# Optimization experiments

Hardware: AMD Instinct MI355X
Metric: run time of the kernel (lower is better)

## Reference

```python
import jax, jax.numpy as jnp
import numpy as np

N_NODES = 25000
N_EDGES = 100000
NODE_IN = 8
EDGE_IN = 4
HID = 32


def _glorot(key, shape):
    fan_in, fan_out = shape[0], shape[-1]
    s = jnp.sqrt(2.0 / (fan_in + fan_out))
    return jax.random.normal(key, shape, dtype=jnp.float32) * s


def setup_inputs() -> dict:
    key = jax.random.key(0)
    ks = jax.random.split(key, 16)
    x = jax.random.normal(ks[0], (N_NODES, NODE_IN), dtype=jnp.float32)
    edge_index = jax.random.randint(ks[1], (2, N_EDGES), 0, N_NODES, dtype=jnp.int64)
    edge_attr = jax.random.uniform(ks[2], (N_EDGES, EDGE_IN), dtype=jnp.float32)
    params = {
        # conv1: edge MLP (edge_in -> node_in*hid), root lin (node_in->hid, no bias), bias
        'w_mlp1': _glorot(ks[3], (EDGE_IN, NODE_IN * HID)),
        'b_mlp1': jnp.zeros((NODE_IN * HID,), jnp.float32),
        'root1': _glorot(ks[4], (NODE_IN, HID)),
        'bias1': jnp.zeros((HID,), jnp.float32),
        # conv2
        'w_mlp2': _glorot(ks[5], (EDGE_IN, HID * HID)),
        'b_mlp2': jnp.zeros((HID * HID,), jnp.float32),
        'root2': _glorot(ks[6], (HID, HID)),
        'bias2': jnp.zeros((HID,), jnp.float32),
        # conv3
        'w_mlp3': _glorot(ks[7], (EDGE_IN, HID * HID)),
        'b_mlp3': jnp.zeros((HID * HID,), jnp.float32),
        'root3': _glorot(ks[8], (HID, HID)),
        'bias3': jnp.zeros((HID,), jnp.float32),
        # output head: Linear(hid,hid) -> ReLU -> Linear(hid,1)
        'w_out1': _glorot(ks[9], (HID, HID)),
        'b_out1': jnp.zeros((HID,), jnp.float32),
        'w_out2': _glorot(ks[10], (HID, 1)),
        'b_out2': jnp.zeros((1,), jnp.float32),
    }
    return {'x': x, 'edge_index': edge_index, 'edge_attr': edge_attr, **params}


def _nnconv(x, src, dst, edge_attr, w_mlp, b_mlp, root, bias, in_dim, out_dim, num_nodes):
    # edge MLP -> per-edge weight matrix [E, in, out]
    w_e = jax.nn.relu(edge_attr @ w_mlp + b_mlp).reshape(-1, in_dim, out_dim)
    # gather source features, per-edge matvec
    msg = jnp.einsum('ei,eio->eo', x[src], w_e)  # [E, out]
    # scatter-mean into target nodes
    agg = jax.ops.segment_sum(msg, dst, num_segments=num_nodes)
    cnt = jax.ops.segment_sum(jnp.ones((msg.shape[0],), msg.dtype), dst, num_segments=num_nodes)
    agg = agg / jnp.maximum(cnt, 1.0)[:, None]
    return agg + x @ root + bias


def reference(x, edge_index, edge_attr,
              w_mlp1, b_mlp1, root1, bias1,
              w_mlp2, b_mlp2, root2, bias2,
              w_mlp3, b_mlp3, root3, bias3,
              w_out1, b_out1, w_out2, b_out2):
    src, dst = edge_index[0], edge_index[1]
    n = x.shape[0]
    h = jax.nn.relu(_nnconv(x, src, dst, edge_attr, w_mlp1, b_mlp1, root1, bias1, NODE_IN, HID, n))
    h = jax.nn.relu(_nnconv(h, src, dst, edge_attr, w_mlp2, b_mlp2, root2, bias2, HID, HID, n))
    h = jax.nn.relu(_nnconv(h, src, dst, edge_attr, w_mlp3, b_mlp3, root3, bias3, HID, HID, n))
    h = jax.nn.relu(h @ w_out1 + b_out1)
    return h @ w_out2 + b_out2  # [N, 1]
```

## Files before the change

### kernel.cpp

```cpp
#include <hip/hip_runtime.h>

#define HID 32
#define CAP 64

__global__ __launch_bounds__(256) void build_kernel(
    const int* __restrict__ src, const int* __restrict__ dst,
    const float* __restrict__ ea,
    int* __restrict__ deg, int* __restrict__ perm_src, float4* __restrict__ perm_ea,
    int E)
{
    int e = blockIdx.x * blockDim.x + threadIdx.x;
    if (e >= E) return;
    int d = dst[e];
    int pos = atomicAdd(deg + d, 1) & (CAP - 1);
    size_t slot = (size_t)d * CAP + pos;
    perm_src[slot] = src[e];
    perm_ea[slot]  = *(const float4*)(ea + (size_t)e * 4);
}

__global__ __launch_bounds__(256) void pull8_kernel(
    const float* __restrict__ x,
    const int* __restrict__ deg,
    const int* __restrict__ perm_src, const float4* __restrict__ perm_ea,
    const float* __restrict__ w_mlp,
    const float* __restrict__ b_mlp,
    const float* __restrict__ root,
    const float* __restrict__ bias,
    float* __restrict__ h_out,
    int N)
{
    constexpr int IN = 8, NPG = 4;
    const int o = threadIdx.x & 31;
    const int g = (blockIdx.x * blockDim.x + threadIdx.x) >> 5;
    if (g >= (N + NPG - 1) / NPG) return;

    float wa[IN], wb[IN], wc[IN], wd[IN], br[IN], ro[IN];
    #pragma unroll
    for (int i = 0; i < IN; ++i) {
        int c = i * HID + o;
        wa[i] = w_mlp[c];
        wb[i] = w_mlp[IN * HID + c];
        wc[i] = w_mlp[2 * IN * HID + c];
        wd[i] = w_mlp[3 * IN * HID + c];
        br[i] = b_mlp[c];
        ro[i] = root[c];
    }
    const float bo = bias[o];

    #pragma unroll
    for (int nv = 0; nv < NPG; ++nv) {
        const int v = g * NPG + nv;
        if (v >= N) break;
        const int dg = min(deg[v], CAP);
        const int* ps = perm_src + (size_t)v * CAP;
        const float4* pe = perm_ea + (size_t)v * CAP;

        float acc = 0.f;
        if (dg > 0) {
            int sA = ps[0];
            float4 aA = pe[0];
            for (int k = 0; k < dg; ++k) {
                int sB = 0; float4 aB = make_float4(0.f, 0.f, 0.f, 0.f);
                if (k + 1 < dg) { sB = ps[k + 1]; aB = pe[k + 1]; }
                float4 x0 = *(const float4*)(x + (size_t)sA * IN);
                float4 x1 = *(const float4*)(x + (size_t)sA * IN + 4);
                const float xs[8] = { x0.x, x0.y, x0.z, x0.w, x1.x, x1.y, x1.z, x1.w };
                #pragma unroll
                for (int i = 0; i < IN; ++i) {
                    float t = fmaf(aA.x, wa[i], br[i]);
                    t = fmaf(aA.y, wb[i], t);
                    t = fmaf(aA.z, wc[i], t);
                    t = fmaf(aA.w, wd[i], t);
                    t = fmaxf(t, 0.f);
                    acc = fmaf(xs[i], t, acc);
                }
                sA = sB; aA = aB;
            }
        }
        float4 r0 = *(const float4*)(x + (size_t)v * IN);
        float4 r1 = *(const float4*)(x + (size_t)v * IN + 4);
        const float xr[8] = { r0.x, r0.y, r0.z, r0.w, r1.x, r1.y, r1.z, r1.w };
        float r = bo;
        #pragma unroll
        for (int i = 0; i < IN; ++i) r = fmaf(xr[i], ro[i], r);
        const float m = acc / fmaxf((float)dg, 1.f);
        h_out[(size_t)v * HID + o] = fmaxf(m + r, 0.f);
    }
}

template<bool HEAD>
__global__ __launch_bounds__(256) void pull32_kernel(
    const float* __restrict__ h_in,
    const int* __restrict__ deg,
    const int* __restrict__ perm_src, const float4* __restrict__ perm_ea,
    const float* __restrict__ w_mlp,
    const float* __restrict__ b_mlp,
    const float* __restrict__ root,
    const float* __restrict__ bias,
    const float* __restrict__ hw1, const float* __restrict__ hb1,
    const float* __restrict__ hw2, const float* __restrict__ hb2,
    float* __restrict__ h_out,
    int N)
{
    constexpr int IN = 32, IH = 16, NPW = 5;
    const int lane = threadIdx.x & 63;
    const int o    = lane & 31;
    const int half = lane >> 5;
    const int wave = (blockIdx.x * blockDim.x + threadIdx.x) >> 6;
    if (wave >= (N + NPW - 1) / NPW) return;

    float wa[IH], wb[IH], wc[IH], wd[IH], br[IH], ro[IH];
    #pragma unroll
    for (int i = 0; i < IH; ++i) {
        int c = (half * IH + i) * HID + o;
        wa[i] = w_mlp[c];
        wb[i] = w_mlp[IN * HID + c];
        wc[i] = w_mlp[2 * IN * HID + c];
        wd[i] = w_mlp[3 * IN * HID + c];
        br[i] = b_mlp[c];
        ro[i] = root[c];
    }
    const float bo = bias[o];

    #pragma unroll
    for (int nv = 0; nv < NPW; ++nv) {
        const int v = wave * NPW + nv;
        if (v >= N) break;
        const int dg = min(deg[v], CAP);
        const int* ps = perm_src + (size_t)v * CAP;
        const float4* pe = perm_ea + (size_t)v * CAP;

        float acc = 0.f;
        if (dg > 0) {
            int sA = ps[0];
            float4 aA = pe[0];
            for (int k = 0; k < dg; ++k) {
                int sB = 0; float4 aB = make_float4(0.f, 0.f, 0.f, 0.f);
                if (k + 1 < dg) { sB = ps[k + 1]; aB = pe[k + 1]; }
                const float* xp = h_in + (size_t)sA * IN + half * IH;
                float4 x0 = *(const float4*)(xp);
                float4 x1 = *(const float4*)(xp + 4);
                float4 x2 = *(const float4*)(xp + 8);
                float4 x3 = *(const float4*)(xp + 12);
                const float xs[16] = { x0.x, x0.y, x0.z, x0.w, x1.x, x1.y, x1.z, x1.w,
                                       x2.x, x2.y, x2.z, x2.w, x3.x, x3.y, x3.z, x3.w };
                #pragma unroll
                for (int i = 0; i < IH; ++i) {
                    float t = fmaf(aA.x, wa[i], br[i]);
                    t = fmaf(aA.y, wb[i], t);
                    t = fmaf(aA.z, wc[i], t);
                    t = fmaf(aA.w, wd[i], t);
                    t = fmaxf(t, 0.f);
                    acc = fmaf(xs[i], t, acc);
                }
                sA = sB; aA = aB;
            }
        }
        const float* rp = h_in + (size_t)v * IN + half * IH;
        float4 r0 = *(const float4*)(rp);
        float4 r1 = *(const float4*)(rp + 4);
        float4 r2 = *(const float4*)(rp + 8);
        float4 r3 = *(const float4*)(rp + 12);
        const float xr[16] = { r0.x, r0.y, r0.z, r0.w, r1.x, r1.y, r1.z, r1.w,
                               r2.x, r2.y, r2.z, r2.w, r3.x, r3.y, r3.z, r3.w };
        float rpart = 0.f;
        #pragma unroll
        for (int i = 0; i < IH; ++i) rpart = fmaf(xr[i], ro[i], rpart);

        const float dgf = fmaxf((float)dg, 1.f);
        float part = acc / dgf + rpart;
        part += __shfl_down(part, 32);

        if (lane < 32) {
            float h = fmaxf(part + bo, 0.f);
            if (!HEAD) {
                h_out[(size_t)v * HID + o] = h;
            } else {
                float t = hb1[o];
                #pragma unroll
                for (int i = 0; i < HID; ++i)
                    t = fmaf(__shfl(h, i, 32), hw1[i * HID + o], t);
                t = fmaxf(t, 0.f) * hw2[o];
                #pragma unroll
                for (int dd = 16; dd > 0; dd >>= 1)
                    t += __shfl_down(t, dd, 32);
                if (o == 0) h_out[v] = t + hb2[0];
            }
        }
    }
}

extern "C" void kernel_launch(void* const* d_in, const int* in_sizes, int n_in,
                              void* d_out, int out_size, void* d_ws, size_t ws_size,
                              hipStream_t stream)
{
    const float* x      = (const float*)d_in[0];
    const int*   ei     = (const int*)d_in[1];
    const float* ea     = (const float*)d_in[2];
    const float* w_mlp1 = (const float*)d_in[3];
    const float* b_mlp1 = (const float*)d_in[4];
    const float* root1  = (const float*)d_in[5];
    const float* bias1  = (const float*)d_in[6];
    const float* w_mlp2 = (const float*)d_in[7];
    const float* b_mlp2 = (const float*)d_in[8];
    const float* root2  = (const float*)d_in[9];
    const float* bias2  = (const float*)d_in[10];
    const float* w_mlp3 = (const float*)d_in[11];
    const float* b_mlp3 = (const float*)d_in[12];
    const float* root3  = (const float*)d_in[13];
    const float* bias3  = (const float*)d_in[14];
    const float* w_out1 = (const float*)d_in[15];
    const float* b_out1 = (const float*)d_in[16];
    const float* w_out2 = (const float*)d_in[17];
    const float* b_out2 = (const float*)d_in[18];

    const int NODE_IN = 8;
    const int N = in_sizes[0] / NODE_IN;
    const int E = in_sizes[2] / 4;
    const int* src = ei;
    const int* dst = ei + E;

    char* ws = (char*)d_ws;
    size_t off = 0;
    auto carve = [&](size_t bytes) {
        char* p = ws + off;
        off += (bytes + 255) & ~(size_t)255;
        return p;
    };
    int*    deg      = (int*)carve((size_t)N * 4);
    int*    perm_src = (int*)carve((size_t)N * CAP * 4);
    float4* perm_ea  = (float4*)carve((size_t)N * CAP * 16);
    float*  h1       = (float*)carve((size_t)N * HID * 4);
    float*  h2       = (float*)carve((size_t)N * HID * 4);
    float*  outp     = (float*)d_out;

    const int TB = 256;
    const int buildBlocks = (E + TB - 1) / TB;
    const int NPG = 4, NPW = 5;
    const int p8Blocks  = (((N + NPG - 1) / NPG) * 32 + TB - 1) / TB;
    const int p32Blocks = (((N + NPW - 1) / NPW) * 64 + TB - 1) / TB;

    hipMemsetAsync(deg, 0, (size_t)N * 4, stream);

    build_kernel<<<buildBlocks, TB, 0, stream>>>(src, dst, ea, deg, perm_src, perm_ea, E);

    pull8_kernel<<<p8Blocks, TB, 0, stream>>>(x, deg, perm_src, perm_ea,
                                              w_mlp1, b_mlp1, root1, bias1, h1, N);

    pull32_kernel<false><<<p32Blocks, TB, 0, stream>>>(h1, deg, perm_src, perm_ea,
                                                       w_mlp2, b_mlp2, root2, bias2,
                                                       nullptr, nullptr, nullptr, nullptr, h2, N);

    pull32_kernel<true><<<p32Blocks, TB, 0, stream>>>(h2, deg, perm_src, perm_ea,
                                                      w_mlp3, b_mlp3, root3, bias3,
                                                      w_out1, b_out1, w_out2, b_out2, outp, N);
}
```

Measured before the change: 244.3 us.

## Batch neighbor gathers four at a time and prefetch next node's edge slots

```diff
diff --git a/kernel.cpp b/kernel.cpp
--- a/kernel.cpp
+++ b/kernel.cpp
@@ -1,7 +1,7 @@
 #include <hip/hip_runtime.h>
 
 #define HID 32
-#define CAP 64
+#define CAP 32
 
 __global__ __launch_bounds__(256) void build_kernel(
     const int* __restrict__ src, const int* __restrict__ dst,
@@ -18,7 +18,7 @@
     perm_ea[slot]  = *(const float4*)(ea + (size_t)e * 4);
 }
 
-__global__ __launch_bounds__(256) void pull8_kernel(
+__global__ __launch_bounds__(256, 3) void pull8_kernel(
     const float* __restrict__ x,
     const int* __restrict__ deg,
     const int* __restrict__ perm_src, const float4* __restrict__ perm_ea,
@@ -30,9 +30,10 @@
     int N)
 {
     constexpr int IN = 8, NPG = 4;
-    const int o = threadIdx.x & 31;
-    const int g = (blockIdx.x * blockDim.x + threadIdx.x) >> 5;
-    if (g >= (N + NPG - 1) / NPG) return;
+    const int o  = threadIdx.x & 31;
+    const int g  = (blockIdx.x * blockDim.x + threadIdx.x) >> 5;
+    const int v0 = g * NPG;
+    if (v0 >= N) return;
 
     float wa[IN], wb[IN], wc[IN], wd[IN], br[IN], ro[IN];
     #pragma unroll
@@ -47,49 +48,113 @@
     }
     const float bo = bias[o];
 
+    int dgs[NPG];
+    #pragma unroll
+    for (int t = 0; t < NPG; ++t)
+        dgs[t] = (v0 + t < N) ? min(deg[v0 + t], CAP) : 0;
+
+    int4 s4A = *(const int4*)(perm_src + (size_t)v0 * CAP);
+    float4 aA0 = perm_ea[(size_t)v0 * CAP + 0];
+    float4 aA1 = perm_ea[(size_t)v0 * CAP + 1];
+    float4 aA2 = perm_ea[(size_t)v0 * CAP + 2];
+    float4 aA3 = perm_ea[(size_t)v0 * CAP + 3];
+
     #pragma unroll
     for (int nv = 0; nv < NPG; ++nv) {
-        const int v = g * NPG + nv;
+        const int v = v0 + nv;
         if (v >= N) break;
-        const int dg = min(deg[v], CAP);
-        const int* ps = perm_src + (size_t)v * CAP;
-        const float4* pe = perm_ea + (size_t)v * CAP;
+        const int dg = dgs[nv];
+
+        int ss[4] = { s4A.x, s4A.y, s4A.z, s4A.w };
+        #pragma unroll
+        for (int j = 0; j < 4; ++j) if (j >= dg) ss[j] = 0;
+
+        float4 xg[4][2];
+        #pragma unroll
+        for (int j = 0; j < 4; ++j) {
+            const float* xp = x + (size_t)ss[j] * IN;
+            xg[j][0] = *(const float4*)(xp);
+            xg[j][1] = *(const float4*)(xp + 4);
+        }
+        const float* rp = x + (size_t)v * IN;
+        float4 r0 = *(const float4*)(rp), r1 = *(const float4*)(rp + 4);
+
+        int4 s4B = make_int4(0, 0, 0, 0);
+        float4 aB0 = make_float4(0,0,0,0), aB1 = aB0, aB2 = aB0, aB3 = aB0;
+        if (nv + 1 < NPG && v + 1 < N) {
+            s4B = *(const int4*)(perm_src + (size_t)(v + 1) * CAP);
+            aB0 = perm_ea[(size_t)(v + 1) * CAP + 0];
+            aB1 = perm_ea[(size_t)(v + 1) * CAP + 1];
+            aB2 = perm_ea[(size_t)(v + 1) * CAP + 2];
+            aB3 = perm_ea[(size_t)(v + 1) * CAP + 3];
+        }
 
         float acc = 0.f;
-        if (dg > 0) {
-            int sA = ps[0];
-            float4 aA = pe[0];
-            for (int k = 0; k < dg; ++k) {
-                int sB = 0; float4 aB = make_float4(0.f, 0.f, 0.f, 0.f);
-                if (k + 1 < dg) { sB = ps[k + 1]; aB = pe[k + 1]; }
-                float4 x0 = *(const float4*)(x + (size_t)sA * IN);
-                float4 x1 = *(const float4*)(x + (size_t)sA * IN + 4);
-                const float xs[8] = { x0.x, x0.y, x0.z, x0.w, x1.x, x1.y, x1.z, x1.w };
+        const float4 aa[4] = { aA0, aA1, aA2, aA3 };
+        #pragma unroll
+        for (int j = 0; j < 4; ++j) {
+            if (j < dg) {
                 #pragma unroll
-                for (int i = 0; i < IN; ++i) {
-                    float t = fmaf(aA.x, wa[i], br[i]);
-                    t = fmaf(aA.y, wb[i], t);
-                    t = fmaf(aA.z, wc[i], t);
-                    t = fmaf(aA.w, wd[i], t);
-                    t = fmaxf(t, 0.f);
-                    acc = fmaf(xs[i], t, acc);
+                for (int q = 0; q < 2; ++q) {
+                    const float xs[4] = { xg[j][q].x, xg[j][q].y, xg[j][q].z, xg[j][q].w };
+                    #pragma unroll
+                    for (int j2 = 0; j2 < 4; ++j2) {
+                        const int i = q * 4 + j2;
+                        float t = fmaf(aa[j].x, wa[i], br[i]);
+                        t = fmaf(aa[j].y, wb[i], t);
+                        t = fmaf(aa[j].z, wc[i], t);
+                        t = fmaf(aa[j].w, wd[i], t);
+                        acc = fmaf(xs[j2], fmaxf(t, 0.f), acc);
+                    }
                 }
-                sA = sB; aA = aB;
-            }
-        }
-        float4 r0 = *(const float4*)(x + (size_t)v * IN);
-        float4 r1 = *(const float4*)(x + (size_t)v * IN + 4);
+            }
+        }
+        for (int k0 = 4; k0 < dg; k0 += 4) {
+            int4 s4 = *(const int4*)(perm_src + (size_t)v * CAP + k0);
+            int st[4] = { s4.x, s4.y, s4.z, s4.w };
+            #pragma unroll
+            for (int j = 0; j < 4; ++j) if (k0 + j >= dg) st[j] = 0;
+            float4 ae[4];
+            #pragma unroll
+            for (int j = 0; j < 4; ++j) ae[j] = perm_ea[(size_t)v * CAP + k0 + j];
+            float4 xh[4][2];
+            #pragma unroll
+            for (int j = 0; j < 4; ++j) {
+                const float* xp = x + (size_t)st[j] * IN;
+                xh[j][0] = *(const float4*)(xp);
+                xh[j][1] = *(const float4*)(xp + 4);
+            }
+            #pragma unroll
+            for (int j = 0; j < 4; ++j) {
+                if (k0 + j < dg) {
+                    #pragma unroll
+                    for (int q = 0; q < 2; ++q) {
+                        const float xs[4] = { xh[j][q].x, xh[j][q].y, xh[j][q].z, xh[j][q].w };
+                        #pragma unroll
+                        for (int j2 = 0; j2 < 4; ++j2) {
+                            const int i = q * 4 + j2;
+                            float t = fmaf(ae[j].x, wa[i], br[i]);
+                            t = fmaf(ae[j].y, wb[i], t);
+                            t = fmaf(ae[j].z, wc[i], t);
+                            t = fmaf(ae[j].w, wd[i], t);
+                            acc = fmaf(xs[j2], fmaxf(t, 0.f), acc);
+                        }
+                    }
+                }
+            }
+        }
         const float xr[8] = { r0.x, r0.y, r0.z, r0.w, r1.x, r1.y, r1.z, r1.w };
         float r = bo;
         #pragma unroll
         for (int i = 0; i < IN; ++i) r = fmaf(xr[i], ro[i], r);
-        const float m = acc / fmaxf((float)dg, 1.f);
-        h_out[(size_t)v * HID + o] = fmaxf(m + r, 0.f);
+        h_out[(size_t)v * HID + o] = fmaxf(acc / fmaxf((float)dg, 1.f) + r, 0.f);
+
+        s4A = s4B; aA0 = aB0; aA1 = aB1; aA2 = aB2; aA3 = aB3;
     }
 }
 
 template<bool HEAD>
-__global__ __launch_bounds__(256) void pull32_kernel(
+__global__ __launch_bounds__(256, 2) void pull32_kernel(
     const float* __restrict__ h_in,
     const int* __restrict__ deg,
     const int* __restrict__ perm_src, const float4* __restrict__ perm_ea,
@@ -102,12 +167,13 @@
     float* __restrict__ h_out,
     int N)
 {
-    constexpr int IN = 32, IH = 16, NPW = 5;
+    constexpr int IN = 32, IH = 16, NPW = 4;
     const int lane = threadIdx.x & 63;
     const int o    = lane & 31;
     const int half = lane >> 5;
     const int wave = (blockIdx.x * blockDim.x + threadIdx.x) >> 6;
-    if (wave >= (N + NPW - 1) / NPW) return;
+    const int v0   = wave * NPW;
+    if (v0 >= N) return;
 
     float wa[IH], wb[IH], wc[IH], wd[IH], br[IH], ro[IH];
     #pragma unroll
@@ -122,53 +188,114 @@
     }
     const float bo = bias[o];
 
+    int dgs[NPW];
+    #pragma unroll
+    for (int t = 0; t < NPW; ++t)
+        dgs[t] = (v0 + t < N) ? min(deg[v0 + t], CAP) : 0;
+
+    int4 s4A = *(const int4*)(perm_src + (size_t)v0 * CAP);
+    float4 aA0 = perm_ea[(size_t)v0 * CAP + 0];
+    float4 aA1 = perm_ea[(size_t)v0 * CAP + 1];
+    float4 aA2 = perm_ea[(size_t)v0 * CAP + 2];
+    float4 aA3 = perm_ea[(size_t)v0 * CAP + 3];
+
     #pragma unroll
     for (int nv = 0; nv < NPW; ++nv) {
-        const int v = wave * NPW + nv;
+        const int v = v0 + nv;
         if (v >= N) break;
-        const int dg = min(deg[v], CAP);
-        const int* ps = perm_src + (size_t)v * CAP;
-        const float4* pe = perm_ea + (size_t)v * CAP;
+        const int dg = dgs[nv];
+
+        int ss[4] = { s4A.x, s4A.y, s4A.z, s4A.w };
+        #pragma unroll
+        for (int j = 0; j < 4; ++j) if (j >= dg) ss[j] = 0;
+
+        float4 xg[4][4];
+        #pragma unroll
+        for (int j = 0; j < 4; ++j) {
+            const float* xp = h_in + (size_t)ss[j] * IN + half * IH;
+            xg[j][0] = *(const float4*)(xp);
+            xg[j][1] = *(const float4*)(xp + 4);
+            xg[j][2] = *(const float4*)(xp + 8);
+            xg[j][3] = *(const float4*)(xp + 12);
+        }
+        const float* rp = h_in + (size_t)v * IN + half * IH;
+        float4 r0 = *(const float4*)(rp), r1 = *(const float4*)(rp + 4);
+        float4 r2 = *(const float4*)(rp + 8), r3 = *(const float4*)(rp + 12);
+
+        int4 s4B = make_int4(0, 0, 0, 0);
+        float4 aB0 = make_float4(0,0,0,0), aB1 = aB0, aB2 = aB0, aB3 = aB0;
+        if (nv + 1 < NPW && v + 1 < N) {
+            s4B = *(const int4*)(perm_src + (size_t)(v + 1) * CAP);
+            aB0 = perm_ea[(size_t)(v + 1) * CAP + 0];
+            aB1 = perm_ea[(size_t)(v + 1) * CAP + 1];
+            aB2 = perm_ea[(size_t)(v + 1) * CAP + 2];
+            aB3 = perm_ea[(size_t)(v + 1) * CAP + 3];
+        }
 
         float acc = 0.f;
-        if (dg > 0) {
-            int sA = ps[0];
-            float4 aA = pe[0];
-            for (int k = 0; k < dg; ++k) {
-                int sB = 0; float4 aB = make_float4(0.f, 0.f, 0.f, 0.f);
-                if (k + 1 < dg) { sB = ps[k + 1]; aB = pe[k + 1]; }
-                const float* xp = h_in + (size_t)sA * IN + half * IH;
-                float4 x0 = *(const float4*)(xp);
-                float4 x1 = *(const float4*)(xp + 4);
-                float4 x2 = *(const float4*)(xp + 8);
-                float4 x3 = *(const float4*)(xp + 12);
-                const float xs[16] = { x0.x, x0.y, x0.z, x0.w, x1.x, x1.y, x1.z, x1.w,
-                                       x2.x, x2.y, x2.z, x2.w, x3.x, x3.y, x3.z, x3.w };
+        const float4 aa[4] = { aA0, aA1, aA2, aA3 };
+        #pragma unroll
+        for (int j = 0; j < 4; ++j) {
+            if (j < dg) {
                 #pragma unroll
-                for (int i = 0; i < IH; ++i) {
-                    float t = fmaf(aA.x, wa[i], br[i]);
-                    t = fmaf(aA.y, wb[i], t);
-                    t = fmaf(aA.z, wc[i], t);
-                    t = fmaf(aA.w, wd[i], t);
-                    t = fmaxf(t, 0.f);
-                    acc = fmaf(xs[i], t, acc);
+                for (int q = 0; q < 4; ++q) {
+                    const float xs[4] = { xg[j][q].x, xg[j][q].y, xg[j][q].z, xg[j][q].w };
+                    #pragma unroll
+                    for (int j2 = 0; j2 < 4; ++j2) {
+                        const int i = q * 4 + j2;
+                        float t = fmaf(aa[j].x, wa[i], br[i]);
+                        t = fmaf(aa[j].y, wb[i], t);
+                        t = fmaf(aa[j].z, wc[i], t);
+                        t = fmaf(aa[j].w, wd[i], t);
+                        acc = fmaf(xs[j2], fmaxf(t, 0.f), acc);
+                    }
                 }
-                sA = sB; aA = aB;
-            }
-        }
-        const float* rp = h_in + (size_t)v * IN + half * IH;
-        float4 r0 = *(const float4*)(rp);
-        float4 r1 = *(const float4*)(rp + 4);
-        float4 r2 = *(const float4*)(rp + 8);
-        float4 r3 = *(const float4*)(rp + 12);
+            }
+        }
+        for (int k0 = 4; k0 < dg; k0 += 4) {
+            int4 s4 = *(const int4*)(perm_src + (size_t)v * CAP + k0);
+            int st[4] = { s4.x, s4.y, s4.z, s4.w };
+            #pragma unroll
+            for (int j = 0; j < 4; ++j) if (k0 + j >= dg) st[j] = 0;
+            float4 ae[4];
+            #pragma unroll
+            for (int j = 0; j < 4; ++j) ae[j] = perm_ea[(size_t)v * CAP + k0 + j];
+            float4 xh[4][4];
+            #pragma unroll
+            for (int j = 0; j < 4; ++j) {
+                const float* xp = h_in + (size_t)st[j] * IN + half * IH;
+                xh[j][0] = *(const float4*)(xp);
+                xh[j][1] = *(const float4*)(xp + 4);
+                xh[j][2] = *(const float4*)(xp + 8);
+                xh[j][3] = *(const float4*)(xp + 12);
+            }
+            #pragma unroll
+            for (int j = 0; j < 4; ++j) {
+                if (k0 + j < dg) {
+                    #pragma unroll
+                    for (int q = 0; q < 4; ++q) {
+                        const float xs[4] = { xh[j][q].x, xh[j][q].y, xh[j][q].z, xh[j][q].w };
+                        #pragma unroll
+                        for (int j2 = 0; j2 < 4; ++j2) {
+                            const int i = q * 4 + j2;
+                            float t = fmaf(ae[j].x, wa[i], br[i]);
+                            t = fmaf(ae[j].y, wb[i], t);
+                            t = fmaf(ae[j].z, wc[i], t);
+                            t = fmaf(ae[j].w, wd[i], t);
+                            acc = fmaf(xs[j2], fmaxf(t, 0.f), acc);
+                        }
+                    }
+                }
+            }
+        }
+
         const float xr[16] = { r0.x, r0.y, r0.z, r0.w, r1.x, r1.y, r1.z, r1.w,
                                r2.x, r2.y, r2.z, r2.w, r3.x, r3.y, r3.z, r3.w };
         float rpart = 0.f;
         #pragma unroll
         for (int i = 0; i < IH; ++i) rpart = fmaf(xr[i], ro[i], rpart);
 
-        const float dgf = fmaxf((float)dg, 1.f);
-        float part = acc / dgf + rpart;
+        float part = acc / fmaxf((float)dg, 1.f) + rpart;
         part += __shfl_down(part, 32);
 
         if (lane < 32) {
@@ -187,6 +314,8 @@
                 if (o == 0) h_out[v] = t + hb2[0];
             }
         }
+
+        s4A = s4B; aA0 = aB0; aA1 = aB1; aA2 = aB2; aA3 = aB3;
     }
 }
 
@@ -236,7 +365,7 @@
 
     const int TB = 256;
     const int buildBlocks = (E + TB - 1) / TB;
-    const int NPG = 4, NPW = 5;
+    const int NPG = 4, NPW = 4;
     const int p8Blocks  = (((N + NPG - 1) / NPG) * 32 + TB - 1) / TB;
     const int p32Blocks = (((N + NPW - 1) / NPW) * 64 + TB - 1) / TB;
 
```

New measurement: 219.3 us. -10.3%, faster.

## Stage edge-MLP weights in LDS, batch four edge gathers, shrink slot capacity

Applied to the files above, without the earlier changes.

```diff
diff --git a/kernel.cpp b/kernel.cpp
--- a/kernel.cpp
+++ b/kernel.cpp
@@ -1,7 +1,9 @@
 #include <hip/hip_runtime.h>
 
 #define HID 32
-#define CAP 64
+#define CAP 32
+#define WPAD 20
+#define PSTRIDE 1280
 
 __global__ __launch_bounds__(256) void build_kernel(
     const int* __restrict__ src, const int* __restrict__ dst,
@@ -18,7 +20,24 @@
     perm_ea[slot]  = *(const float4*)(ea + (size_t)e * 4);
 }
 
-__global__ __launch_bounds__(256) void pull8_kernel(
+__device__ __forceinline__ float edge_quad(const float4 av, const float4 xv,
+                                           const float4 WA, const float4 WB,
+                                           const float4 WC, const float4 WD,
+                                           const float4 BR, float acc)
+{
+    float t;
+    t = fmaf(av.x, WA.x, BR.x); t = fmaf(av.y, WB.x, t); t = fmaf(av.z, WC.x, t); t = fmaf(av.w, WD.x, t);
+    acc = fmaf(xv.x, fmaxf(t, 0.f), acc);
+    t = fmaf(av.x, WA.y, BR.y); t = fmaf(av.y, WB.y, t); t = fmaf(av.z, WC.y, t); t = fmaf(av.w, WD.y, t);
+    acc = fmaf(xv.y, fmaxf(t, 0.f), acc);
+    t = fmaf(av.x, WA.z, BR.z); t = fmaf(av.y, WB.z, t); t = fmaf(av.z, WC.z, t); t = fmaf(av.w, WD.z, t);
+    acc = fmaf(xv.z, fmaxf(t, 0.f), acc);
+    t = fmaf(av.x, WA.w, BR.w); t = fmaf(av.y, WB.w, t); t = fmaf(av.z, WC.w, t); t = fmaf(av.w, WD.w, t);
+    acc = fmaf(xv.w, fmaxf(t, 0.f), acc);
+    return acc;
+}
+
+__global__ __launch_bounds__(256, 4) void pull8_kernel(
     const float* __restrict__ x,
     const int* __restrict__ deg,
     const int* __restrict__ perm_src, const float4* __restrict__ perm_ea,
@@ -29,67 +48,60 @@
     float* __restrict__ h_out,
     int N)
 {
-    constexpr int IN = 8, NPG = 4;
-    const int o = threadIdx.x & 31;
-    const int g = (blockIdx.x * blockDim.x + threadIdx.x) >> 5;
-    if (g >= (N + NPG - 1) / NPG) return;
-
-    float wa[IN], wb[IN], wc[IN], wd[IN], br[IN], ro[IN];
-    #pragma unroll
-    for (int i = 0; i < IN; ++i) {
-        int c = i * HID + o;
-        wa[i] = w_mlp[c];
-        wb[i] = w_mlp[IN * HID + c];
-        wc[i] = w_mlp[2 * IN * HID + c];
-        wd[i] = w_mlp[3 * IN * HID + c];
-        br[i] = b_mlp[c];
-        ro[i] = root[c];
-    }
+    constexpr int IN = 8, NPG = 8;
+    const int lane = threadIdx.x & 63;
+    const int o = lane & 31, half = lane >> 5;
+    const int wave = (blockIdx.x * blockDim.x + threadIdx.x) >> 6;
+    const int v0 = wave * NPG;
+    if (v0 >= N) return;
+
+    const int cb = half * 4 * HID + o;
+    const float4 WA = make_float4(w_mlp[cb],       w_mlp[cb+32],       w_mlp[cb+64],       w_mlp[cb+96]);
+    const float4 WB = make_float4(w_mlp[256+cb],   w_mlp[256+cb+32],   w_mlp[256+cb+64],   w_mlp[256+cb+96]);
+    const float4 WC = make_float4(w_mlp[512+cb],   w_mlp[512+cb+32],   w_mlp[512+cb+64],   w_mlp[512+cb+96]);
+    const float4 WD = make_float4(w_mlp[768+cb],   w_mlp[768+cb+32],   w_mlp[768+cb+64],   w_mlp[768+cb+96]);
+    const float4 BR = make_float4(b_mlp[cb],       b_mlp[cb+32],       b_mlp[cb+64],       b_mlp[cb+96]);
+    const float4 RO = make_float4(root[cb],        root[cb+32],        root[cb+64],        root[cb+96]);
     const float bo = bias[o];
 
-    #pragma unroll
     for (int nv = 0; nv < NPG; ++nv) {
-        const int v = g * NPG + nv;
+        const int v = v0 + nv;
         if (v >= N) break;
-        const int dg = min(deg[v], CAP);
+        const int dt = deg[v];
+        const int dg = min(dt, CAP);
         const int* ps = perm_src + (size_t)v * CAP;
         const float4* pe = perm_ea + (size_t)v * CAP;
 
         float acc = 0.f;
-        if (dg > 0) {
-            int sA = ps[0];
-            float4 aA = pe[0];
-            for (int k = 0; k < dg; ++k) {
-                int sB = 0; float4 aB = make_float4(0.f, 0.f, 0.f, 0.f);
-                if (k + 1 < dg) { sB = ps[k + 1]; aB = pe[k + 1]; }
-                float4 x0 = *(const float4*)(x + (size_t)sA * IN);
-                float4 x1 = *(const float4*)(x + (size_t)sA * IN + 4);
-                const float xs[8] = { x0.x, x0.y, x0.z, x0.w, x1.x, x1.y, x1.z, x1.w };
-                #pragma unroll
-                for (int i = 0; i < IN; ++i) {
-                    float t = fmaf(aA.x, wa[i], br[i]);
-                    t = fmaf(aA.y, wb[i], t);
-                    t = fmaf(aA.z, wc[i], t);
-                    t = fmaf(aA.w, wd[i], t);
-                    t = fmaxf(t, 0.f);
-                    acc = fmaf(xs[i], t, acc);
-                }
-                sA = sB; aA = aB;
-            }
-        }
-        float4 r0 = *(const float4*)(x + (size_t)v * IN);
-        float4 r1 = *(const float4*)(x + (size_t)v * IN + 4);
-        const float xr[8] = { r0.x, r0.y, r0.z, r0.w, r1.x, r1.y, r1.z, r1.w };
-        float r = bo;
-        #pragma unroll
-        for (int i = 0; i < IN; ++i) r = fmaf(xr[i], ro[i], r);
-        const float m = acc / fmaxf((float)dg, 1.f);
-        h_out[(size_t)v * HID + o] = fmaxf(m + r, 0.f);
+        for (int k0 = 0; k0 < dg; k0 += 4) {
+            int4 s4 = *(const int4*)(ps + k0);
+            int ss[4] = { s4.x, s4.y, s4.z, s4.w };
+            float4 aa[4];
+            #pragma unroll
+            for (int j = 0; j < 4; ++j) {
+                aa[j] = pe[k0 + j];
+                if (k0 + j >= dg) ss[j] = 0;
+            }
+            float4 xg[4];
+            #pragma unroll
+            for (int j = 0; j < 4; ++j)
+                xg[j] = *(const float4*)(x + (size_t)ss[j] * IN + half * 4);
+            #pragma unroll
+            for (int j = 0; j < 4; ++j)
+                if (k0 + j < dg)
+                    acc = edge_quad(aa[j], xg[j], WA, WB, WC, WD, BR, acc);
+        }
+        const float4 xr = *(const float4*)(x + (size_t)v * IN + half * 4);
+        float rpart = fmaf(xr.x, RO.x, fmaf(xr.y, RO.y, fmaf(xr.z, RO.z, xr.w * RO.w)));
+        float part = acc / fmaxf((float)dt, 1.f) + rpart;
+        part += __shfl_down(part, 32);
+        if (lane < 32)
+            h_out[(size_t)v * HID + o] = fmaxf(part + bo, 0.f);
     }
 }
 
 template<bool HEAD>
-__global__ __launch_bounds__(256) void pull32_kernel(
+__global__ __launch_bounds__(256, 4) void pull32_kernel(
     const float* __restrict__ h_in,
     const int* __restrict__ deg,
     const int* __restrict__ perm_src, const float4* __restrict__ perm_ea,
@@ -102,89 +114,104 @@
     float* __restrict__ h_out,
     int N)
 {
-    constexpr int IN = 32, IH = 16, NPW = 5;
+    constexpr int IN = 32, NPW = 8;
+    __shared__ __align__(16) float lw[8768];
+    for (int t = threadIdx.x; t < 4096; t += 256) {
+        int c = t >> 10, rem = t & 1023, i = rem >> 5, oo = rem & 31;
+        lw[((c * 2 + (i >> 4)) * 32 + oo) * WPAD + (i & 15)] = w_mlp[t];
+    }
+    for (int t = threadIdx.x; t < 1024; t += 256) {
+        int i = t >> 5, oo = t & 31;
+        lw[((8  + (i >> 4)) * 32 + oo) * WPAD + (i & 15)] = b_mlp[t];
+        lw[((10 + (i >> 4)) * 32 + oo) * WPAD + (i & 15)] = root[t];
+    }
+    if (HEAD) {
+        for (int t = threadIdx.x; t < 1024; t += 256) lw[7680 + t] = hw1[t];
+        if (threadIdx.x < 32) {
+            lw[8704 + threadIdx.x] = hb1[threadIdx.x];
+            lw[8736 + threadIdx.x] = hw2[threadIdx.x];
+        }
+    }
+    __syncthreads();
+
     const int lane = threadIdx.x & 63;
-    const int o    = lane & 31;
-    const int half = lane >> 5;
+    const int o = lane & 31, half = lane >> 5;
     const int wave = (blockIdx.x * blockDim.x + threadIdx.x) >> 6;
-    if (wave >= (N + NPW - 1) / NPW) return;
-
-    float wa[IH], wb[IH], wc[IH], wd[IH], br[IH], ro[IH];
-    #pragma unroll
-    for (int i = 0; i < IH; ++i) {
-        int c = (half * IH + i) * HID + o;
-        wa[i] = w_mlp[c];
-        wb[i] = w_mlp[IN * HID + c];
-        wc[i] = w_mlp[2 * IN * HID + c];
-        wd[i] = w_mlp[3 * IN * HID + c];
-        br[i] = b_mlp[c];
-        ro[i] = root[c];
-    }
+    const int v0 = wave * NPW;
+    if (v0 >= N) return;
+
+    const float* wp = lw + ((half << 5) + o) * WPAD;
     const float bo = bias[o];
-
-    #pragma unroll
+    float hb2v = 0.f;
+    if (HEAD) hb2v = hb2[0];
+
     for (int nv = 0; nv < NPW; ++nv) {
-        const int v = wave * NPW + nv;
+        const int v = v0 + nv;
         if (v >= N) break;
-        const int dg = min(deg[v], CAP);
+        const int dt = deg[v];
+        const int dg = min(dt, CAP);
         const int* ps = perm_src + (size_t)v * CAP;
         const float4* pe = perm_ea + (size_t)v * CAP;
 
         float acc = 0.f;
-        if (dg > 0) {
-            int sA = ps[0];
-            float4 aA = pe[0];
-            for (int k = 0; k < dg; ++k) {
-                int sB = 0; float4 aB = make_float4(0.f, 0.f, 0.f, 0.f);
-                if (k + 1 < dg) { sB = ps[k + 1]; aB = pe[k + 1]; }
-                const float* xp = h_in + (size_t)sA * IN + half * IH;
-                float4 x0 = *(const float4*)(xp);
-                float4 x1 = *(const float4*)(xp + 4);
-                float4 x2 = *(const float4*)(xp + 8);
-                float4 x3 = *(const float4*)(xp + 12);
-                const float xs[16] = { x0.x, x0.y, x0.z, x0.w, x1.x, x1.y, x1.z, x1.w,
-                                       x2.x, x2.y, x2.z, x2.w, x3.x, x3.y, x3.z, x3.w };
+        for (int k0 = 0; k0 < dg; k0 += 4) {
+            int4 s4 = *(const int4*)(ps + k0);
+            int ss[4] = { s4.x, s4.y, s4.z, s4.w };
+            float4 aa[4];
+            #pragma unroll
+            for (int j = 0; j < 4; ++j) {
+                aa[j] = pe[k0 + j];
+                if (k0 + j >= dg) ss[j] = 0;
+            }
+            float4 xg[4][4];
+            #pragma unroll
+            for (int j = 0; j < 4; ++j) {
+                const float* xp = h_in + (size_t)ss[j] * IN + (half << 4);
+                xg[j][0] = *(const float4*)(xp);
+                xg[j][1] = *(const float4*)(xp + 4);
+                xg[j][2] = *(const float4*)(xp + 8);
+                xg[j][3] = *(const float4*)(xp + 12);
+            }
+            #pragma unroll
+            for (int k = 0; k < 4; ++k) {
+                const float4 WA = *(const float4*)(wp + 4 * k);
+                const float4 WB = *(const float4*)(wp + PSTRIDE     + 4 * k);
+                const float4 WC = *(const float4*)(wp + 2 * PSTRIDE + 4 * k);
+                const float4 WD = *(const float4*)(wp + 3 * PSTRIDE + 4 * k);
+                const float4 BR = *(const float4*)(wp + 4 * PSTRIDE + 4 * k);
                 #pragma unroll
-                for (int i = 0; i < IH; ++i) {
-                    float t = fmaf(aA.x, wa[i], br[i]);
-                    t = fmaf(aA.y, wb[i], t);
-                    t = fmaf(aA.z, wc[i], t);
-                    t = fmaf(aA.w, wd[i], t);
-                    t = fmaxf(t, 0.f);
-                    acc = fmaf(xs[i], t, acc);
-                }
-                sA = sB; aA = aB;
-            }
-        }
-        const float* rp = h_in + (size_t)v * IN + half * IH;
-        float4 r0 = *(const float4*)(rp);
-        float4 r1 = *(const float4*)(rp + 4);
-        float4 r2 = *(const float4*)(rp + 8);
-        float4 r3 = *(const float4*)(rp + 12);
-        const float xr[16] = { r0.x, r0.y, r0.z, r0.w, r1.x, r1.y, r1.z, r1.w,
-                               r2.x, r2.y, r2.z, r2.w, r3.x, r3.y, r3.z, r3.w };
+                for (int j = 0; j < 4; ++j)
+                    if (k0 + j < dg)
+                        acc = edge_quad(aa[j], xg[j][k], WA, WB, WC, WD, BR, acc);
+            }
+        }
+        const float* rp = h_in + (size_t)v * IN + (half << 4);
         float rpart = 0.f;
         #pragma unroll
-        for (int i = 0; i < IH; ++i) rpart = fmaf(xr[i], ro[i], rpart);
-
-        const float dgf = fmaxf((float)dg, 1.f);
-        float part = acc / dgf + rpart;
+        for (int k = 0; k < 4; ++k) {
+            const float4 RO = *(const float4*)(wp + 5 * PSTRIDE + 4 * k);
+            const float4 xr = *(const float4*)(rp + 4 * k);
+            rpart = fmaf(xr.x, RO.x, rpart);
+            rpart = fmaf(xr.y, RO.y, rpart);
+            rpart = fmaf(xr.z, RO.z, rpart);
+            rpart = fmaf(xr.w, RO.w, rpart);
+        }
+        float part = acc / fmaxf((float)dt, 1.f) + rpart;
         part += __shfl_down(part, 32);
-
         if (lane < 32) {
             float h = fmaxf(part + bo, 0.f);
             if (!HEAD) {
                 h_out[(size_t)v * HID + o] = h;
             } else {
-                float t = hb1[o];
+                float tt = lw[8704 + o];
                 #pragma unroll
                 for (int i = 0; i < HID; ++i)
-                    t = fmaf(__shfl(h, i, 32), hw1[i * HID + o], t);
-                t = fmaxf(t, 0.f) * hw2[o];
+                    tt = fmaf(__shfl(h, i, 32), lw[7680 + i * 32 + o], tt);
+                tt = fmaxf(tt, 0.f) * lw[8736 + o];
                 #pragma unroll
                 for (int dd = 16; dd > 0; dd >>= 1)
-                    t += __shfl_down(t, dd, 32);
-                if (o == 0) h_out[v] = t + hb2[0];
+                    tt += __shfl_down(tt, dd, 32);
+                if (o == 0) h_out[v] = tt + hb2v;
             }
         }
     }
@@ -236,22 +263,20 @@
 
     const int TB = 256;
     const int buildBlocks = (E + TB - 1) / TB;
-    const int NPG = 4, NPW = 5;
-    const int p8Blocks  = (((N + NPG - 1) / NPG) * 32 + TB - 1) / TB;
-    const int p32Blocks = (((N + NPW - 1) / NPW) * 64 + TB - 1) / TB;
+    const int pullBlocks = (N + 31) / 32;
 
     hipMemsetAsync(deg, 0, (size_t)N * 4, stream);
 
     build_kernel<<<buildBlocks, TB, 0, stream>>>(src, dst, ea, deg, perm_src, perm_ea, E);
 
-    pull8_kernel<<<p8Blocks, TB, 0, stream>>>(x, deg, perm_src, perm_ea,
-                                              w_mlp1, b_mlp1, root1, bias1, h1, N);
-
-    pull32_kernel<false><<<p32Blocks, TB, 0, stream>>>(h1, deg, perm_src, perm_ea,
-                                                       w_mlp2, b_mlp2, root2, bias2,
-                                                       nullptr, nullptr, nullptr, nullptr, h2, N);
-
-    pull32_kernel<true><<<p32Blocks, TB, 0, stream>>>(h2, deg, perm_src, perm_ea,
-                                                      w_mlp3, b_mlp3, root3, bias3,
-                                                      w_out1, b_out1, w_out2, b_out2, outp, N);
-}
+    pull8_kernel<<<pullBlocks, TB, 0, stream>>>(x, deg, perm_src, perm_ea,
+                                                w_mlp1, b_mlp1, root1, bias1, h1, N);
+
+    pull32_kernel<false><<<pullBlocks, TB, 0, stream>>>(h1, deg, perm_src, perm_ea,
+                                                        w_mlp2, b_mlp2, root2, bias2,
+                                                        nullptr, nullptr, nullptr, nullptr, h2, N);
+
+    pull32_kernel<true><<<pullBlocks, TB, 0, stream>>>(h2, deg, perm_src, perm_ea,
+                                                       w_mlp3, b_mlp3, root3, bias3,
+                                                       w_out1, b_out1, w_out2, b_out2, outp, N);
+}
```

New measurement: 412.2 us. 1.69x slower.
